# Performance work log

Hardware: AMD Instinct MI355X
Metric: run time of the kernel (lower is better)

Reference implementation:

```python
import jax, jax.numpy as jnp
import numpy as np

N_A, N_P, N_T = 40000, 100000, 20000
D = 128
OUT = 64
E_AP, E_PT = 500000, 800000


def setup_inputs() -> dict:
    key = jax.random.key(0)
    ks = jax.random.split(key, 24)
    s = 1.0 / np.sqrt(D)
    inp = {
        'x_author': jax.random.normal(ks[0], (N_A, D), jnp.float32),
        'x_paper': jax.random.normal(ks[1], (N_P, D), jnp.float32),
        'x_term': jax.random.normal(ks[2], (N_T, D), jnp.float32),
        'W_l': jax.random.normal(ks[3], (3, 2, 4, D, D), jnp.float32) * s,
        'b_l': jax.random.normal(ks[4], (3, 2, 4, D), jnp.float32) * 0.01,
        'W_r': jax.random.normal(ks[5], (3, 2, 4, D, D), jnp.float32) * s,
        'lin_model_W': jax.random.normal(ks[6], (D, OUT), jnp.float32) * s,
        'lin_model_b': jax.random.normal(ks[7], (OUT,), jnp.float32) * 0.01,
        'lin_temp_W': jax.random.normal(ks[8], (D, OUT), jnp.float32) * s,
        'lin_temp_b': jax.random.normal(ks[9], (OUT,), jnp.float32) * 0.01,
        'lin2_W': jax.random.normal(ks[10], (OUT, 1), jnp.float32) * (1.0 / np.sqrt(OUT)),
        'lin2_b': jnp.ones((1,), jnp.float32),
        'src_ap': jax.random.randint(ks[11], (E_AP,), 0, N_A, jnp.int32),
        'dst_ap': jax.random.randint(ks[12], (E_AP,), 0, N_P, jnp.int32),
        'src_pa': jax.random.randint(ks[13], (E_AP,), 0, N_P, jnp.int32),
        'dst_pa': jax.random.randint(ks[14], (E_AP,), 0, N_A, jnp.int32),
        'src_pt': jax.random.randint(ks[15], (E_PT,), 0, N_P, jnp.int32),
        'dst_pt': jax.random.randint(ks[16], (E_PT,), 0, N_T, jnp.int32),
        'src_tp': jax.random.randint(ks[17], (E_PT,), 0, N_T, jnp.int32),
        'dst_tp': jax.random.randint(ks[18], (E_PT,), 0, N_P, jnp.int32),
    }
    return inp


def _sage(x_src, x_dst, src, dst, n_dst, Wl, bl, Wr):
    # PyG SAGEConv: lin_l(mean_aggr(x_j)) + lin_r(x_dst); lin_r has no bias.
    xj = x_src[src]                                         # [E, D] gather
    ssum = jax.ops.segment_sum(xj, dst, num_segments=n_dst)  # [n_dst, D]
    cnt = jax.ops.segment_sum(jnp.ones((src.shape[0],), x_src.dtype), dst,
                              num_segments=n_dst)
    mean = ssum / jnp.maximum(cnt, 1.0)[:, None]
    return mean @ Wl + bl + x_dst @ Wr


def _hetero_stack(xa, xp, xt, Wl, bl, Wr, edges, relu=True):
    # Wl/bl/Wr: [num_layers, 4, ...]; relation order: a->p, p->a, p->t, t->p.
    (sap, dap, spa, dpa, spt, dpt, stp, dtp) = edges
    n_layers = Wl.shape[0]
    for l in range(n_layers):
        p_new = (_sage(xa, xp, sap, dap, N_P, Wl[l, 0], bl[l, 0], Wr[l, 0])
                 + _sage(xt, xp, stp, dtp, N_P, Wl[l, 3], bl[l, 3], Wr[l, 3]))
        a_new = _sage(xp, xa, spa, dpa, N_A, Wl[l, 1], bl[l, 1], Wr[l, 1])
        t_new = _sage(xp, xt, spt, dpt, N_T, Wl[l, 2], bl[l, 2], Wr[l, 2])
        xa, xp, xt = jax.nn.relu(a_new), jax.nn.relu(p_new), jax.nn.relu(t_new)
    return xa, xp, xt


def reference(x_author, x_paper, x_term, W_l, b_l, W_r,
              lin_model_W, lin_model_b, lin_temp_W, lin_temp_b,
              lin2_W, lin2_b,
              src_ap, dst_ap, src_pa, dst_pa, src_pt, dst_pt, src_tp, dst_tp):
    edges = (src_ap, dst_ap, src_pa, dst_pa, src_pt, dst_pt, src_tp, dst_tp)
    # stack 0: self.model (DBLP) on raw features
    ma, mp, mt = _hetero_stack(x_author, x_paper, x_term,
                               W_l[0], b_l[0], W_r[0], edges)
    logits = ma @ lin_model_W + lin_model_b                  # [N_A, OUT]
    # stack 1: graph_temperature_scale (DBLP) on model's hidden x_dict
    ta, tp_, tt = _hetero_stack(ma, mp, mt, W_l[1], b_l[1], W_r[1], edges)
    ll1 = ta @ lin_temp_W + lin_temp_b                       # [N_A, OUT]
    temperature = ll1 @ lin2_W + lin2_b                      # [N_A, 1]
    # stack 2: self.convs on raw features (dropout = identity in eval mode)
    oa, op, ot = _hetero_stack(x_author, x_paper, x_term,
                               W_l[2], b_l[2], W_r[2], edges)
    return logits / temperature, oa, op, ot
```

## Files before the change

### kernel.cpp

```cpp
#include <hip/hip_runtime.h>
#include <cstdint>

#define N_A 40000
#define N_P 100000
#define N_T 20000
#define D 128
#define OUT_DIM 64
#define E_AP 500000
#define E_PT 800000

typedef __attribute__((ext_vector_type(8))) short bf16x8;
typedef __attribute__((ext_vector_type(4))) float f32x4;

static inline int ceil_div(int a, int b){ return (a + b - 1) / b; }

__device__ inline unsigned short f2bf(float f){
  uint32_t u = __builtin_bit_cast(uint32_t, f);
  uint32_t r = (u + 0x7FFFu + ((u >> 16) & 1u)) >> 16;
  return (unsigned short)r;
}
__device__ inline float bf2f(unsigned short h){
  uint32_t u = ((uint32_t)h) << 16;
  return __builtin_bit_cast(float, u);
}

__global__ void hist_kernel(const int* __restrict__ dst, int E, int* __restrict__ cnt){
  int i = blockIdx.x * blockDim.x + threadIdx.x;
  if (i < E) atomicAdd(&cnt[dst[i]], 1);
}

__global__ void block_sums_kernel(const int* __restrict__ cnt, int n, int* __restrict__ bsums){
  __shared__ int red[256];
  int b = blockIdx.x, t = threadIdx.x;
  int base = b * 1024;
  int s = 0;
  for (int i = t; i < 1024; i += 256){ int idx = base + i; if (idx < n) s += cnt[idx]; }
  red[t] = s; __syncthreads();
  for (int off = 128; off > 0; off >>= 1){ if (t < off) red[t] += red[t + off]; __syncthreads(); }
  if (t == 0) bsums[b] = red[0];
}

__global__ void scan_bsums_kernel(int* bsums, int nb){
  __shared__ int sh[128];
  int t = threadIdx.x;
  int v = (t < nb) ? bsums[t] : 0;
  sh[t] = v; __syncthreads();
  int inc = v;
  for (int off = 1; off < 128; off <<= 1){
    int x = (t >= off) ? sh[t - off] : 0; __syncthreads();
    inc += x; sh[t] = inc; __syncthreads();
  }
  if (t < nb) bsums[t] = inc - v;
}

__global__ void scan_final_kernel(const int* __restrict__ cnt, int n, const int* __restrict__ bsums,
                                  int* __restrict__ rowptr, int E){
  __shared__ int sh[256];
  int b = blockIdx.x, t = threadIdx.x;
  int base = b * 1024 + t * 4;
  int v[4]; int s = 0;
  #pragma unroll
  for (int j = 0; j < 4; j++){ int idx = base + j; v[j] = (idx < n) ? cnt[idx] : 0; s += v[j]; }
  sh[t] = s; __syncthreads();
  int inc = s;
  for (int off = 1; off < 256; off <<= 1){
    int x = (t >= off) ? sh[t - off] : 0; __syncthreads();
    inc += x; sh[t] = inc; __syncthreads();
  }
  int run = inc - s + bsums[b];
  #pragma unroll
  for (int j = 0; j < 4; j++){ int idx = base + j; if (idx < n) rowptr[idx] = run; run += v[j]; }
  if (b == 0 && t == 0) rowptr[n] = E;
}

__global__ void cursor_inv_kernel(const int* __restrict__ rowptr, const int* __restrict__ cnt,
                                  int n, int* __restrict__ cursor, float* __restrict__ inv){
  int i = blockIdx.x * blockDim.x + threadIdx.x;
  if (i < n){
    cursor[i] = rowptr[i];
    int c = cnt[i];
    inv[i] = 1.0f / (float)(c > 0 ? c : 1);
  }
}

__global__ void fill_kernel(const int* __restrict__ src, const int* __restrict__ dst, int E,
                            int* __restrict__ cursor, int* __restrict__ eidx){
  int i = blockIdx.x * blockDim.x + threadIdx.x;
  if (i < E){
    int d = dst[i];
    int pos = atomicAdd(&cursor[d], 1);
    eidx[pos] = src[i];
  }
}

__global__ void combine_wr_kernel(const float* __restrict__ Wr, float* __restrict__ wrc){
  int i = blockIdx.x * blockDim.x + threadIdx.x;
  if (i < 6 * D * D){
    int sl = i >> 14; int off = i & (D * D - 1);
    wrc[i] = Wr[(size_t)(sl * 4 + 0) * D * D + off] + Wr[(size_t)(sl * 4 + 3) * D * D + off];
  }
}

__global__ void combine_bias_kernel(const float* __restrict__ bl, float* __restrict__ bcomb){
  int i = blockIdx.x * blockDim.x + threadIdx.x;
  if (i < 6 * D){
    int sl = i >> 7; int off = i & (D - 1);
    bcomb[i] = bl[(size_t)(sl * 4 + 0) * D + off] + bl[(size_t)(sl * 4 + 3) * D + off];
  }
}

__global__ __launch_bounds__(256)
void pack_weights_kernel(const float* __restrict__ W_l, const float* __restrict__ W_r,
                         const float* __restrict__ wrc, const float* __restrict__ linW,
                         unsigned short* __restrict__ packs){
  int id = blockIdx.x;
  const float* src; int N = 128;
  if (id < 24)      src = W_l + (size_t)id * 16384;
  else if (id < 48) src = W_r + (size_t)(id - 24) * 16384;
  else if (id < 54) src = wrc + (size_t)(id - 48) * 16384;
  else            { src = linW; N = 64; }
  unsigned short* dhi = packs + (size_t)id * 32768;
  unsigned short* dlo = dhi + 16384;
  int ncf = N / 16;
  int slots = 4 * ncf * 64;
  for (int s = threadIdx.x; s < slots; s += 256){
    int frag = s >> 6, l = s & 63;
    int kc = frag / ncf, cf = frag - kc * ncf;
    int kb = kc * 32 + ((l >> 4) * 8);
    int col = cf * 16 + (l & 15);
    bf16x8 hv, lv;
    #pragma unroll
    for (int i = 0; i < 8; ++i){
      float f = src[(size_t)(kb + i) * N + col];
      unsigned short h = f2bf(f);
      hv[i] = (short)h;
      lv[i] = (short)f2bf(f - bf2f(h));
    }
    *(bf16x8*)(dhi + (size_t)s * 8) = hv;
    *(bf16x8*)(dlo + (size_t)s * 8) = lv;
  }
}

__global__ __launch_bounds__(256)
void agg_mean_kernel(const int* __restrict__ rowptr, const int* __restrict__ eidx,
                     const float* __restrict__ inv, const float* __restrict__ xsrc,
                     float* __restrict__ out, int ndst){
  int w = (blockIdx.x * blockDim.x + threadIdx.x) >> 6;
  if (w >= ndst) return;
  int l = threadIdx.x & 63;
  int p = l >> 5, kk = l & 31;
  int beg = rowptr[w], end = rowptr[w + 1];
  float4 a0 = make_float4(0,0,0,0), a1 = make_float4(0,0,0,0);
  float4 a2 = make_float4(0,0,0,0), a3 = make_float4(0,0,0,0);
  int e = beg;
  for (; e + 8 <= end; e += 8){
    int s0 = eidx[e + p], s1 = eidx[e + 2 + p], s2 = eidx[e + 4 + p], s3 = eidx[e + 6 + p];
    float4 v0 = ((const float4*)(xsrc + (size_t)s0 * D))[kk];
    float4 v1 = ((const float4*)(xsrc + (size_t)s1 * D))[kk];
    float4 v2 = ((const float4*)(xsrc + (size_t)s2 * D))[kk];
    float4 v3 = ((const float4*)(xsrc + (size_t)s3 * D))[kk];
    a0.x += v0.x; a0.y += v0.y; a0.z += v0.z; a0.w += v0.w;
    a1.x += v1.x; a1.y += v1.y; a1.z += v1.z; a1.w += v1.w;
    a2.x += v2.x; a2.y += v2.y; a2.z += v2.z; a2.w += v2.w;
    a3.x += v3.x; a3.y += v3.y; a3.z += v3.z; a3.w += v3.w;
  }
  if (e + 4 <= end){
    int s0 = eidx[e + p], s1 = eidx[e + 2 + p];
    float4 v0 = ((const float4*)(xsrc + (size_t)s0 * D))[kk];
    float4 v1 = ((const float4*)(xsrc + (size_t)s1 * D))[kk];
    a0.x += v0.x; a0.y += v0.y; a0.z += v0.z; a0.w += v0.w;
    a1.x += v1.x; a1.y += v1.y; a1.z += v1.z; a1.w += v1.w;
    e += 4;
  }
  if (e + 2 <= end){
    int s0 = eidx[e + p];
    float4 v0 = ((const float4*)(xsrc + (size_t)s0 * D))[kk];
    a0.x += v0.x; a0.y += v0.y; a0.z += v0.z; a0.w += v0.w;
    e += 2;
  }
  if (e < end && p == 0){
    int s0 = eidx[e];
    float4 v0 = ((const float4*)(xsrc + (size_t)s0 * D))[kk];
    a0.x += v0.x; a0.y += v0.y; a0.z += v0.z; a0.w += v0.w;
  }
  a0.x += a1.x + a2.x + a3.x; a0.y += a1.y + a2.y + a3.y;
  a0.z += a1.z + a2.z + a3.z; a0.w += a1.w + a2.w + a3.w;
  a0.x += __shfl_xor(a0.x, 32); a0.y += __shfl_xor(a0.y, 32);
  a0.z += __shfl_xor(a0.z, 32); a0.w += __shfl_xor(a0.w, 32);
  if (p == 0){
    float iv = inv[w];
    float4 r; r.x = a0.x * iv; r.y = a0.y * iv; r.z = a0.z * iv; r.w = a0.w * iv;
    ((float4*)(out + (size_t)w * D))[kk] = r;
  }
}

template<int NIN, int NCFT, bool RELU, bool DIV>
__global__ __launch_bounds__(256)
void gemm_mfma(const float* __restrict__ in0, const unsigned short* hi0, const unsigned short* lo0,
               const float* __restrict__ in1, const unsigned short* hi1, const unsigned short* lo1,
               const float* __restrict__ in2, const unsigned short* hi2, const unsigned short* lo2,
               const float* __restrict__ bias, const float* __restrict__ tdiv,
               float* __restrict__ out, int nrows){
  constexpr int WC = NCFT / 4;
  constexpr int WR = 4 / WC;
  const int tid    = threadIdx.x;
  const int w      = tid >> 6;
  const int l      = tid & 63;
  const int lane15 = l & 15;
  const int colg   = l >> 4;
  const int wr     = w / WC, wc = w % WC;
  const int rbase  = blockIdx.x * (WR * 64) + wr * 64;

  f32x4 acc[4][4];
  #pragma unroll
  for (int m = 0; m < 4; ++m)
    #pragma unroll
    for (int cf = 0; cf < 4; ++cf) acc[m][cf] = (f32x4){0.f, 0.f, 0.f, 0.f};

  const float* ins[3]          = {in0, in1, in2};
  const unsigned short* his[3] = {hi0, hi1, hi2};
  const unsigned short* los[3] = {lo0, lo1, lo2};

  #pragma unroll
  for (int inp = 0; inp < NIN; ++inp){
    const float* A = ins[inp];
    const bf16x8* WH = (const bf16x8*)his[inp];
    const bf16x8* WL = (const bf16x8*)los[inp];
    #pragma unroll
    for (int kc = 0; kc < 4; ++kc){
      bf16x8 bh[4], bl[4];
      #pragma unroll
      for (int cf = 0; cf < 4; ++cf){
        int idx = (kc * NCFT + wc * 4 + cf) * 64 + l;
        bh[cf] = WH[idx];
        bl[cf] = WL[idx];
      }
      bf16x8 ah[4], al[4];
      #pragma unroll
      for (int m = 0; m < 4; ++m){
        int gr = rbase + m * 16 + lane15; if (gr >= nrows) gr = nrows - 1;
        const float4* p = (const float4*)(A + (size_t)gr * 128 + kc * 32 + colg * 8);
        float4 v0 = p[0], v1 = p[1];
        float fs[8] = {v0.x, v0.y, v0.z, v0.w, v1.x, v1.y, v1.z, v1.w};
        #pragma unroll
        for (int i = 0; i < 8; ++i){
          uint32_t u = __builtin_bit_cast(uint32_t, fs[i]);
          unsigned short h = (unsigned short)(u >> 16);
          float r = fs[i] - __builtin_bit_cast(float, u & 0xFFFF0000u);
          ah[m][i] = (short)h;
          al[m][i] = (short)(__builtin_bit_cast(uint32_t, r) >> 16);
        }
      }
      #pragma unroll
      for (int cf = 0; cf < 4; ++cf){
        #pragma unroll
        for (int m = 0; m < 4; ++m){
          acc[m][cf] = __builtin_amdgcn_mfma_f32_16x16x32_bf16(ah[m], bh[cf], acc[m][cf], 0, 0, 0);
          acc[m][cf] = __builtin_amdgcn_mfma_f32_16x16x32_bf16(al[m], bh[cf], acc[m][cf], 0, 0, 0);
          acc[m][cf] = __builtin_amdgcn_mfma_f32_16x16x32_bf16(ah[m], bl[cf], acc[m][cf], 0, 0, 0);
        }
      }
    }
  }

  #pragma unroll
  for (int cf = 0; cf < 4; ++cf){
    int col = (wc * 4 + cf) * 16 + lane15;
    float bv = bias[col];
    #pragma unroll
    for (int m = 0; m < 4; ++m){
      #pragma unroll
      for (int i = 0; i < 4; ++i){
        int gr = rbase + m * 16 + colg * 4 + i;
        if (gr < nrows){
          float v = acc[m][cf][i] + bv;
          if (RELU) v = fmaxf(v, 0.f);
          if (DIV)  v = v / tdiv[gr];
          out[(size_t)gr * (NCFT * 16) + col] = v;
        }
      }
    }
  }
}

__global__ void wtc_kernel(const float* __restrict__ Wt, const float* __restrict__ bt,
                           const float* __restrict__ W2, const float* __restrict__ b2,
                           float* __restrict__ wtc){
  int k = threadIdx.x;
  if (k < 128){
    float s = 0.f;
    #pragma unroll 4
    for (int j = 0; j < 64; ++j) s += Wt[k * 64 + j] * W2[j];
    wtc[k] = s;
  }
  if (k == 0){
    float s = 0.f;
    for (int j = 0; j < 64; ++j) s += bt[j] * W2[j];
    wtc[128] = s + b2[0];
  }
}

__global__ __launch_bounds__(256)
void temp_kernel(const float* __restrict__ ta, const float* __restrict__ wtc,
                 float* __restrict__ temp, int n){
  int w = (blockIdx.x * blockDim.x + threadIdx.x) >> 6;
  if (w >= n) return;
  int l = threadIdx.x & 63;
  float2 v = ((const float2*)(ta + (size_t)w * D))[l];
  float2 c = ((const float2*)wtc)[l];
  float s = v.x * c.x + v.y * c.y;
  #pragma unroll
  for (int off = 32; off > 0; off >>= 1) s += __shfl_xor(s, off);
  if (l == 0) temp[w] = s + wtc[128];
}

extern "C" void kernel_launch(void* const* d_in, const int* in_sizes, int n_in,
                              void* d_out, int out_size, void* d_ws, size_t ws_size,
                              hipStream_t stream){
  const float* x_author    = (const float*)d_in[0];
  const float* x_paper     = (const float*)d_in[1];
  const float* x_term      = (const float*)d_in[2];
  const float* W_l         = (const float*)d_in[3];
  const float* b_l         = (const float*)d_in[4];
  const float* W_r         = (const float*)d_in[5];
  const float* lin_model_W = (const float*)d_in[6];
  const float* lin_model_b = (const float*)d_in[7];
  const float* lin_temp_W  = (const float*)d_in[8];
  const float* lin_temp_b  = (const float*)d_in[9];
  const float* lin2_W      = (const float*)d_in[10];
  const float* lin2_b      = (const float*)d_in[11];
  const int* src_ap = (const int*)d_in[12];
  const int* dst_ap = (const int*)d_in[13];
  const int* src_pa = (const int*)d_in[14];
  const int* dst_pa = (const int*)d_in[15];
  const int* src_pt = (const int*)d_in[16];
  const int* dst_pt = (const int*)d_in[17];
  const int* src_tp = (const int*)d_in[18];
  const int* dst_tp = (const int*)d_in[19];

  char* wp = (char*)d_ws;
  auto alloc = [&](size_t bytes)->void*{
    void* r = (void*)wp; wp += (bytes + 255) & ~(size_t)255; return r;
  };
  int*   rowptr_ap = (int*)alloc((N_P + 1) * 4);
  int*   cnt_ap    = (int*)alloc(N_P * 4);
  int*   cur_ap    = (int*)alloc(N_P * 4);
  int*   eidx_ap   = (int*)alloc((size_t)E_AP * 4);
  float* inv_ap    = (float*)alloc(N_P * 4);
  int*   rowptr_pa = (int*)alloc((N_A + 1) * 4);
  int*   cnt_pa    = (int*)alloc(N_A * 4);
  int*   cur_pa    = (int*)alloc(N_A * 4);
  int*   eidx_pa   = (int*)alloc((size_t)E_AP * 4);
  float* inv_pa    = (float*)alloc(N_A * 4);
  int*   rowptr_pt = (int*)alloc((N_T + 1) * 4);
  int*   cnt_pt    = (int*)alloc(N_T * 4);
  int*   cur_pt    = (int*)alloc(N_T * 4);
  int*   eidx_pt   = (int*)alloc((size_t)E_PT * 4);
  float* inv_pt    = (float*)alloc(N_T * 4);
  int*   rowptr_tp = (int*)alloc((N_P + 1) * 4);
  int*   cnt_tp    = (int*)alloc(N_P * 4);
  int*   cur_tp    = (int*)alloc(N_P * 4);
  int*   eidx_tp   = (int*)alloc((size_t)E_PT * 4);
  float* inv_tp    = (float*)alloc(N_P * 4);
  int*   bsums     = (int*)alloc(1024 * 4);
  unsigned short* packs = (unsigned short*)alloc((size_t)55 * 32768 * 2);
  float* wrc   = (float*)alloc((size_t)6 * D * D * 4);
  float* bcomb = (float*)alloc((size_t)6 * D * 4);
  float* wtc   = (float*)alloc(129 * 4);
  float* temp  = (float*)alloc((size_t)N_A * 4);
  float* gA  = (float*)alloc((size_t)N_A * D * 4);
  float* gP1 = (float*)alloc((size_t)N_P * D * 4);
  float* gP2 = (float*)alloc((size_t)N_P * D * 4);
  float* gT  = (float*)alloc((size_t)N_T * D * 4);
  float* A1 = (float*)alloc((size_t)N_A * D * 4);
  float* P1 = (float*)alloc((size_t)N_P * D * 4);
  float* T1 = (float*)alloc((size_t)N_T * D * 4);
  float* A2 = (float*)alloc((size_t)N_A * D * 4);
  float* P2 = (float*)alloc((size_t)N_P * D * 4);
  float* T2 = (float*)alloc((size_t)N_T * D * 4);
  float* A0 = A2;
  float* P0 = P2;
  float* T0 = T2;
  float* TA = P2;

  auto build = [&](const int* src, const int* dst, int E, int n,
                   int* rowptr, int* cnt, int* cursor, int* eidx, float* inv){
    hipMemsetAsync(cnt, 0, (size_t)n * 4, stream);
    hist_kernel<<<ceil_div(E, 256), 256, 0, stream>>>(dst, E, cnt);
    int nb = ceil_div(n, 1024);
    block_sums_kernel<<<nb, 256, 0, stream>>>(cnt, n, bsums);
    scan_bsums_kernel<<<1, 128, 0, stream>>>(bsums, nb);
    scan_final_kernel<<<nb, 256, 0, stream>>>(cnt, n, bsums, rowptr, E);
    cursor_inv_kernel<<<ceil_div(n, 256), 256, 0, stream>>>(rowptr, cnt, n, cursor, inv);
    fill_kernel<<<ceil_div(E, 256), 256, 0, stream>>>(src, dst, E, cursor, eidx);
  };
  build(src_ap, dst_ap, E_AP, N_P, rowptr_ap, cnt_ap, cur_ap, eidx_ap, inv_ap);
  build(src_pa, dst_pa, E_AP, N_A, rowptr_pa, cnt_pa, cur_pa, eidx_pa, inv_pa);
  build(src_pt, dst_pt, E_PT, N_T, rowptr_pt, cnt_pt, cur_pt, eidx_pt, inv_pt);
  build(src_tp, dst_tp, E_PT, N_P, rowptr_tp, cnt_tp, cur_tp, eidx_tp, inv_tp);

  combine_wr_kernel<<<ceil_div(6 * D * D, 256), 256, 0, stream>>>(W_r, wrc);
  combine_bias_kernel<<<ceil_div(6 * D, 256), 256, 0, stream>>>(b_l, bcomb);
  pack_weights_kernel<<<55, 256, 0, stream>>>(W_l, W_r, wrc, lin_model_W, packs);
  wtc_kernel<<<1, 128, 0, stream>>>(lin_temp_W, lin_temp_b, lin2_W, lin2_b, wtc);

  auto HI = [&](int id){ return packs + (size_t)id * 32768; };
  auto LO = [&](int id){ return packs + (size_t)id * 32768 + 16384; };
  auto IDL = [&](int s, int l, int r){ return (s * 2 + l) * 4 + r; };
  auto IDR = [&](int s, int l, int r){ return 24 + (s * 2 + l) * 4 + r; };
  auto IDC = [&](int s, int l){ return 48 + s * 2 + l; };
  auto Bl  = [&](int s, int l, int r){ return b_l + (size_t)((s * 2 + l) * 4 + r) * D; };
  auto BC  = [&](int s, int l){ return bcomb + (size_t)(s * 2 + l) * D; };

  auto agg = [&](const int* rowptr, const int* eidx, const float* inv,
                 const float* xsrc, float* outp, int ndst){
    agg_mean_kernel<<<ceil_div(ndst, 4), 256, 0, stream>>>(rowptr, eidx, inv, xsrc, outp, ndst);
  };

  auto agg_all = [&](const float* ia, const float* ip, const float* it){
    agg(rowptr_ap, eidx_ap, inv_ap, ia, gP1, N_P);
    agg(rowptr_tp, eidx_tp, inv_tp, it, gP2, N_P);
    agg(rowptr_pa, eidx_pa, inv_pa, ip, gA, N_A);
    agg(rowptr_pt, eidx_pt, inv_pt, ip, gT, N_T);
  };

  auto gemms = [&](const float* ia, const float* ip, const float* it, int s, int l,
                   float* oa, float* op, float* ot){
    if (op) gemm_mfma<3, 8, true, false><<<ceil_div(N_P, 128), 256, 0, stream>>>(
        gP1, HI(IDL(s, l, 0)), LO(IDL(s, l, 0)),
        gP2, HI(IDL(s, l, 3)), LO(IDL(s, l, 3)),
        ip,  HI(IDC(s, l)),    LO(IDC(s, l)),
        BC(s, l), nullptr, op, N_P);
    if (oa) gemm_mfma<2, 8, true, false><<<ceil_div(N_A, 128), 256, 0, stream>>>(
        gA, HI(IDL(s, l, 1)), LO(IDL(s, l, 1)),
        ia, HI(IDR(s, l, 1)), LO(IDR(s, l, 1)),
        nullptr, nullptr, nullptr,
        Bl(s, l, 1), nullptr, oa, N_A);
    if (ot) gemm_mfma<2, 8, true, false><<<ceil_div(N_T, 128), 256, 0, stream>>>(
        gT, HI(IDL(s, l, 2)), LO(IDL(s, l, 2)),
        it, HI(IDR(s, l, 2)), LO(IDR(s, l, 2)),
        nullptr, nullptr, nullptr,
        Bl(s, l, 2), nullptr, ot, N_T);
  };

  float* out_logits = (float*)d_out;
  float* out_oa = out_logits + (size_t)N_A * OUT_DIM;
  float* out_op = out_oa + (size_t)N_A * D;
  float* out_ot = out_op + (size_t)N_P * D;

  agg_all(x_author, x_paper, x_term);
  gemms(x_author, x_paper, x_term, 0, 0, A1, P1, T1);
  gemms(x_author, x_paper, x_term, 2, 0, A2, P2, T2);
  agg_all(A2, P2, T2);
  gemms(A2, P2, T2, 2, 1, out_oa, out_op, out_ot);
  agg_all(A1, P1, T1);
  gemms(A1, P1, T1, 0, 1, A0, P0, T0);
  agg_all(A0, P0, T0);
  gemms(A0, P0, T0, 1, 0, A1, P1, T1);
  agg(rowptr_pa, eidx_pa, inv_pa, P1, gA, N_A);
  gemm_mfma<2, 8, true, false><<<ceil_div(N_A, 128), 256, 0, stream>>>(
      gA, HI(IDL(1, 1, 1)), LO(IDL(1, 1, 1)),
      A1, HI(IDR(1, 1, 1)), LO(IDR(1, 1, 1)),
      nullptr, nullptr, nullptr,
      Bl(1, 1, 1), nullptr, TA, N_A);
  temp_kernel<<<ceil_div(N_A, 4), 256, 0, stream>>>(TA, wtc, temp, N_A);
  gemm_mfma<1, 4, false, true><<<ceil_div(N_A, 256), 256, 0, stream>>>(
      A0, HI(54), LO(54),
      nullptr, nullptr, nullptr,
      nullptr, nullptr, nullptr,
      lin_model_b, temp, out_logits, N_A);
}
```

Baseline: 2.158 ms.

## Store intermediates as split bf16 hi/lo planes and narrow aggregation to 16 lanes

Intermediate activations and aggregated means are now stored as two bf16 planes (hi and residual lo) rather than fp32. The GEMM then loads the MFMA operands directly instead of splitting fp32 values on every tile load. The aggregation kernel now gives each destination row to 16 lanes that each handle 8 columns, and the GEMM row tile per warp (MF) is reduced for the smaller node types. Bytes moved per gather stay the same, since two bf16 planes equal one fp32 row, but they come as two separate 16-byte reads. The hi/lo split also loses a little precision, and the bf16-to-float conversion work moves into the gather loop.

```diff
diff --git a/kernel.cpp b/kernel.cpp
--- a/kernel.cpp
+++ b/kernel.cpp
@@ -22,6 +22,13 @@
 __device__ inline float bf2f(unsigned short h){
   uint32_t u = ((uint32_t)h) << 16;
   return __builtin_bit_cast(float, u);
+}
+__device__ inline uint32_t tsplit_pack(float v){
+  uint32_t u = __builtin_bit_cast(uint32_t, v);
+  uint32_t h = u >> 16;
+  float rem = v - __builtin_bit_cast(float, u & 0xFFFF0000u);
+  uint32_t l = f2bf(rem);
+  return h | (l << 16);
 }
 
 __global__ void hist_kernel(const int* __restrict__ dst, int E, int* __restrict__ cnt){
@@ -141,66 +148,76 @@
   }
 }
 
+__device__ inline void addrow_f32(const float* __restrict__ base, int s, int c, float* acc){
+  const float4* p = (const float4*)(base + (size_t)s * D + c * 8);
+  float4 a = p[0], b = p[1];
+  acc[0] += a.x; acc[1] += a.y; acc[2] += a.z; acc[3] += a.w;
+  acc[4] += b.x; acc[5] += b.y; acc[6] += b.z; acc[7] += b.w;
+}
+__device__ inline void addrow_bf(const unsigned short* __restrict__ H,
+                                 const unsigned short* __restrict__ L, int s, int c, float* acc){
+  bf16x8 h = *(const bf16x8*)(H + (size_t)s * D + c * 8);
+  bf16x8 l = *(const bf16x8*)(L + (size_t)s * D + c * 8);
+  #pragma unroll
+  for (int i = 0; i < 8; ++i)
+    acc[i] += bf2f((unsigned short)h[i]) + bf2f((unsigned short)l[i]);
+}
+
+template<bool SRCF32>
 __global__ __launch_bounds__(256)
 void agg_mean_kernel(const int* __restrict__ rowptr, const int* __restrict__ eidx,
-                     const float* __restrict__ inv, const float* __restrict__ xsrc,
-                     float* __restrict__ out, int ndst){
-  int w = (blockIdx.x * blockDim.x + threadIdx.x) >> 6;
-  if (w >= ndst) return;
-  int l = threadIdx.x & 63;
-  int p = l >> 5, kk = l & 31;
-  int beg = rowptr[w], end = rowptr[w + 1];
-  float4 a0 = make_float4(0,0,0,0), a1 = make_float4(0,0,0,0);
-  float4 a2 = make_float4(0,0,0,0), a3 = make_float4(0,0,0,0);
+                     const float* __restrict__ inv,
+                     const void* __restrict__ srcHv, const void* __restrict__ srcLv,
+                     unsigned short* __restrict__ dstH, unsigned short* __restrict__ dstL,
+                     int ndst){
+  int g = (blockIdx.x * blockDim.x + threadIdx.x) >> 4;
+  if (g >= ndst) return;
+  int c = threadIdx.x & 15;
+  int beg = rowptr[g], end = rowptr[g + 1];
+  float acc[8];
+  #pragma unroll
+  for (int i = 0; i < 8; ++i) acc[i] = 0.f;
+  const float* F = (const float*)srcHv;
+  const unsigned short* H = (const unsigned short*)srcHv;
+  const unsigned short* L = (const unsigned short*)srcLv;
   int e = beg;
-  for (; e + 8 <= end; e += 8){
-    int s0 = eidx[e + p], s1 = eidx[e + 2 + p], s2 = eidx[e + 4 + p], s3 = eidx[e + 6 + p];
-    float4 v0 = ((const float4*)(xsrc + (size_t)s0 * D))[kk];
-    float4 v1 = ((const float4*)(xsrc + (size_t)s1 * D))[kk];
-    float4 v2 = ((const float4*)(xsrc + (size_t)s2 * D))[kk];
-    float4 v3 = ((const float4*)(xsrc + (size_t)s3 * D))[kk];
-    a0.x += v0.x; a0.y += v0.y; a0.z += v0.z; a0.w += v0.w;
-    a1.x += v1.x; a1.y += v1.y; a1.z += v1.z; a1.w += v1.w;
-    a2.x += v2.x; a2.y += v2.y; a2.z += v2.z; a2.w += v2.w;
-    a3.x += v3.x; a3.y += v3.y; a3.z += v3.z; a3.w += v3.w;
-  }
-  if (e + 4 <= end){
-    int s0 = eidx[e + p], s1 = eidx[e + 2 + p];
-    float4 v0 = ((const float4*)(xsrc + (size_t)s0 * D))[kk];
-    float4 v1 = ((const float4*)(xsrc + (size_t)s1 * D))[kk];
-    a0.x += v0.x; a0.y += v0.y; a0.z += v0.z; a0.w += v0.w;
-    a1.x += v1.x; a1.y += v1.y; a1.z += v1.z; a1.w += v1.w;
-    e += 4;
-  }
-  if (e + 2 <= end){
-    int s0 = eidx[e + p];
-    float4 v0 = ((const float4*)(xsrc + (size_t)s0 * D))[kk];
-    a0.x += v0.x; a0.y += v0.y; a0.z += v0.z; a0.w += v0.w;
-    e += 2;
-  }
-  if (e < end && p == 0){
+  for (; e + 4 <= end; e += 4){
+    int s0 = eidx[e], s1 = eidx[e + 1], s2 = eidx[e + 2], s3 = eidx[e + 3];
+    if (SRCF32){
+      addrow_f32(F, s0, c, acc); addrow_f32(F, s1, c, acc);
+      addrow_f32(F, s2, c, acc); addrow_f32(F, s3, c, acc);
+    } else {
+      addrow_bf(H, L, s0, c, acc); addrow_bf(H, L, s1, c, acc);
+      addrow_bf(H, L, s2, c, acc); addrow_bf(H, L, s3, c, acc);
+    }
+  }
+  for (; e < end; ++e){
     int s0 = eidx[e];
-    float4 v0 = ((const float4*)(xsrc + (size_t)s0 * D))[kk];
-    a0.x += v0.x; a0.y += v0.y; a0.z += v0.z; a0.w += v0.w;
-  }
-  a0.x += a1.x + a2.x + a3.x; a0.y += a1.y + a2.y + a3.y;
-  a0.z += a1.z + a2.z + a3.z; a0.w += a1.w + a2.w + a3.w;
-  a0.x += __shfl_xor(a0.x, 32); a0.y += __shfl_xor(a0.y, 32);
-  a0.z += __shfl_xor(a0.z, 32); a0.w += __shfl_xor(a0.w, 32);
-  if (p == 0){
-    float iv = inv[w];
-    float4 r; r.x = a0.x * iv; r.y = a0.y * iv; r.z = a0.z * iv; r.w = a0.w * iv;
-    ((float4*)(out + (size_t)w * D))[kk] = r;
-  }
-}
-
-template<int NIN, int NCFT, bool RELU, bool DIV>
+    if (SRCF32) addrow_f32(F, s0, c, acc);
+    else        addrow_bf(H, L, s0, c, acc);
+  }
+  float iv = inv[g];
+  bf16x8 hv, lv;
+  #pragma unroll
+  for (int i = 0; i < 8; ++i){
+    uint32_t pk = tsplit_pack(acc[i] * iv);
+    hv[i] = (short)(pk & 0xFFFF);
+    lv[i] = (short)(pk >> 16);
+  }
+  *(bf16x8*)(dstH + (size_t)g * D + c * 8) = hv;
+  *(bf16x8*)(dstL + (size_t)g * D + c * 8) = lv;
+}
+
+template<int NIN, int F32MASK, int NCFT, int MF, bool RELU, bool DIV, bool OUT32>
 __global__ __launch_bounds__(256)
-void gemm_mfma(const float* __restrict__ in0, const unsigned short* hi0, const unsigned short* lo0,
-               const float* __restrict__ in1, const unsigned short* hi1, const unsigned short* lo1,
-               const float* __restrict__ in2, const unsigned short* hi2, const unsigned short* lo2,
+void gemm_mfma(const void* __restrict__ aH0, const unsigned short* __restrict__ aL0,
+               const unsigned short* __restrict__ wH0, const unsigned short* __restrict__ wL0,
+               const void* __restrict__ aH1, const unsigned short* __restrict__ aL1,
+               const unsigned short* __restrict__ wH1, const unsigned short* __restrict__ wL1,
+               const void* __restrict__ aH2, const unsigned short* __restrict__ aL2,
+               const unsigned short* __restrict__ wH2, const unsigned short* __restrict__ wL2,
                const float* __restrict__ bias, const float* __restrict__ tdiv,
-               float* __restrict__ out, int nrows){
+               void* __restrict__ outp, size_t out_lo_off, int nrows){
   constexpr int WC = NCFT / 4;
   constexpr int WR = 4 / WC;
   const int tid    = threadIdx.x;
@@ -209,23 +226,23 @@
   const int lane15 = l & 15;
   const int colg   = l >> 4;
   const int wr     = w / WC, wc = w % WC;
-  const int rbase  = blockIdx.x * (WR * 64) + wr * 64;
-
-  f32x4 acc[4][4];
-  #pragma unroll
-  for (int m = 0; m < 4; ++m)
+  const int rbase  = blockIdx.x * (WR * MF * 16) + wr * (MF * 16);
+
+  f32x4 acc[MF][4];
+  #pragma unroll
+  for (int m = 0; m < MF; ++m)
     #pragma unroll
     for (int cf = 0; cf < 4; ++cf) acc[m][cf] = (f32x4){0.f, 0.f, 0.f, 0.f};
 
-  const float* ins[3]          = {in0, in1, in2};
-  const unsigned short* his[3] = {hi0, hi1, hi2};
-  const unsigned short* los[3] = {lo0, lo1, lo2};
+  const void* aHs[3]           = {aH0, aH1, aH2};
+  const unsigned short* aLs[3] = {aL0, aL1, aL2};
+  const unsigned short* wHs[3] = {wH0, wH1, wH2};
+  const unsigned short* wLs[3] = {wL0, wL1, wL2};
 
   #pragma unroll
   for (int inp = 0; inp < NIN; ++inp){
-    const float* A = ins[inp];
-    const bf16x8* WH = (const bf16x8*)his[inp];
-    const bf16x8* WL = (const bf16x8*)los[inp];
+    const bf16x8* WH = (const bf16x8*)wHs[inp];
+    const bf16x8* WL = (const bf16x8*)wLs[inp];
     #pragma unroll
     for (int kc = 0; kc < 4; ++kc){
       bf16x8 bh[4], bl[4];
@@ -235,26 +252,33 @@
         bh[cf] = WH[idx];
         bl[cf] = WL[idx];
       }
-      bf16x8 ah[4], al[4];
+      bf16x8 ah[MF], al[MF];
       #pragma unroll
-      for (int m = 0; m < 4; ++m){
+      for (int m = 0; m < MF; ++m){
         int gr = rbase + m * 16 + lane15; if (gr >= nrows) gr = nrows - 1;
-        const float4* p = (const float4*)(A + (size_t)gr * 128 + kc * 32 + colg * 8);
-        float4 v0 = p[0], v1 = p[1];
-        float fs[8] = {v0.x, v0.y, v0.z, v0.w, v1.x, v1.y, v1.z, v1.w};
-        #pragma unroll
-        for (int i = 0; i < 8; ++i){
-          uint32_t u = __builtin_bit_cast(uint32_t, fs[i]);
-          unsigned short h = (unsigned short)(u >> 16);
-          float r = fs[i] - __builtin_bit_cast(float, u & 0xFFFF0000u);
-          ah[m][i] = (short)h;
-          al[m][i] = (short)(__builtin_bit_cast(uint32_t, r) >> 16);
+        if ((F32MASK >> inp) & 1){
+          const float* Af = (const float*)aHs[inp];
+          const float4* p = (const float4*)(Af + (size_t)gr * 128 + kc * 32 + colg * 8);
+          float4 v0 = p[0], v1 = p[1];
+          float fs[8] = {v0.x, v0.y, v0.z, v0.w, v1.x, v1.y, v1.z, v1.w};
+          #pragma unroll
+          for (int i = 0; i < 8; ++i){
+            uint32_t pk = tsplit_pack(fs[i]);
+            ah[m][i] = (short)(pk & 0xFFFF);
+            al[m][i] = (short)(pk >> 16);
+          }
+        } else {
+          const unsigned short* AH = (const unsigned short*)aHs[inp];
+          const unsigned short* AL = aLs[inp];
+          size_t idx = (size_t)gr * 128 + kc * 32 + colg * 8;
+          ah[m] = *(const bf16x8*)(AH + idx);
+          al[m] = *(const bf16x8*)(AL + idx);
         }
       }
       #pragma unroll
       for (int cf = 0; cf < 4; ++cf){
         #pragma unroll
-        for (int m = 0; m < 4; ++m){
+        for (int m = 0; m < MF; ++m){
           acc[m][cf] = __builtin_amdgcn_mfma_f32_16x16x32_bf16(ah[m], bh[cf], acc[m][cf], 0, 0, 0);
           acc[m][cf] = __builtin_amdgcn_mfma_f32_16x16x32_bf16(al[m], bh[cf], acc[m][cf], 0, 0, 0);
           acc[m][cf] = __builtin_amdgcn_mfma_f32_16x16x32_bf16(ah[m], bl[cf], acc[m][cf], 0, 0, 0);
@@ -268,7 +292,7 @@
     int col = (wc * 4 + cf) * 16 + lane15;
     float bv = bias[col];
     #pragma unroll
-    for (int m = 0; m < 4; ++m){
+    for (int m = 0; m < MF; ++m){
       #pragma unroll
       for (int i = 0; i < 4; ++i){
         int gr = rbase + m * 16 + colg * 4 + i;
@@ -276,7 +300,14 @@
           float v = acc[m][cf][i] + bv;
           if (RELU) v = fmaxf(v, 0.f);
           if (DIV)  v = v / tdiv[gr];
-          out[(size_t)gr * (NCFT * 16) + col] = v;
+          size_t oi = (size_t)gr * (NCFT * 16) + col;
+          if (OUT32){
+            ((float*)outp)[oi] = v;
+          } else {
+            uint32_t pk = tsplit_pack(v);
+            ((unsigned short*)outp)[oi] = (unsigned short)(pk & 0xFFFF);
+            ((unsigned short*)outp)[out_lo_off + oi] = (unsigned short)(pk >> 16);
+          }
         }
       }
     }
@@ -301,18 +332,21 @@
 }
 
 __global__ __launch_bounds__(256)
-void temp_kernel(const float* __restrict__ ta, const float* __restrict__ wtc,
-                 float* __restrict__ temp, int n){
+void temp_kernel(const unsigned short* __restrict__ taH, const unsigned short* __restrict__ taL,
+                 const float* __restrict__ wtc, float* __restrict__ temp, int n){
   int w = (blockIdx.x * blockDim.x + threadIdx.x) >> 6;
   if (w >= n) return;
   int l = threadIdx.x & 63;
-  float2 v = ((const float2*)(ta + (size_t)w * D))[l];
+  ushort2 h = *(const ushort2*)(taH + (size_t)w * D + 2 * l);
+  ushort2 lo = *(const ushort2*)(taL + (size_t)w * D + 2 * l);
   float2 c = ((const float2*)wtc)[l];
-  float s = v.x * c.x + v.y * c.y;
+  float s = (bf2f(h.x) + bf2f(lo.x)) * c.x + (bf2f(h.y) + bf2f(lo.y)) * c.y;
   #pragma unroll
   for (int off = 32; off > 0; off >>= 1) s += __shfl_xor(s, off);
   if (l == 0) temp[w] = s + wtc[128];
 }
+
+struct Split { unsigned short* h; unsigned short* l; };
 
 extern "C" void kernel_launch(void* const* d_in, const int* in_sizes, int n_in,
                               void* d_out, int out_size, void* d_ws, size_t ws_size,
@@ -341,6 +375,10 @@
   char* wp = (char*)d_ws;
   auto alloc = [&](size_t bytes)->void*{
     void* r = (void*)wp; wp += (bytes + 255) & ~(size_t)255; return r;
+  };
+  auto mkSplit = [&](int n)->Split{
+    unsigned short* p = (unsigned short*)alloc((size_t)n * D * 4);
+    return {p, p + (size_t)n * D};
   };
   int*   rowptr_ap = (int*)alloc((N_P + 1) * 4);
   int*   cnt_ap    = (int*)alloc(N_P * 4);
@@ -368,24 +406,15 @@
   float* bcomb = (float*)alloc((size_t)6 * D * 4);
   float* wtc   = (float*)alloc(129 * 4);
   float* temp  = (float*)alloc((size_t)N_A * 4);
-  float* gA  = (float*)alloc((size_t)N_A * D * 4);
-  float* gP1 = (float*)alloc((size_t)N_P * D * 4);
-  float* gP2 = (float*)alloc((size_t)N_P * D * 4);
-  float* gT  = (float*)alloc((size_t)N_T * D * 4);
-  float* A1 = (float*)alloc((size_t)N_A * D * 4);
-  float* P1 = (float*)alloc((size_t)N_P * D * 4);
-  float* T1 = (float*)alloc((size_t)N_T * D * 4);
-  float* A2 = (float*)alloc((size_t)N_A * D * 4);
-  float* P2 = (float*)alloc((size_t)N_P * D * 4);
-  float* T2 = (float*)alloc((size_t)N_T * D * 4);
-  float* A0 = A2;
-  float* P0 = P2;
-  float* T0 = T2;
-  float* TA = P2;
+  Split gA = mkSplit(N_A), gP1 = mkSplit(N_P), gP2 = mkSplit(N_P), gT = mkSplit(N_T);
+  Split A1 = mkSplit(N_A), P1 = mkSplit(N_P), T1 = mkSplit(N_T);
+  Split A2 = mkSplit(N_A), P2 = mkSplit(N_P), T2 = mkSplit(N_T);
+  Split A0 = A2, P0 = P2, T0 = T2;
+  Split TA = P2;
 
   auto build = [&](const int* src, const int* dst, int E, int n,
                    int* rowptr, int* cnt, int* cursor, int* eidx, float* inv){
-    hipMemsetAsync(cnt, 0, (size_t)n * 4, stream);
+    (void)hipMemsetAsync(cnt, 0, (size_t)n * 4, stream);
     hist_kernel<<<ceil_div(E, 256), 256, 0, stream>>>(dst, E, cnt);
     int nb = ceil_div(n, 1024);
     block_sums_kernel<<<nb, 256, 0, stream>>>(cnt, n, bsums);
@@ -412,35 +441,81 @@
   auto Bl  = [&](int s, int l, int r){ return b_l + (size_t)((s * 2 + l) * 4 + r) * D; };
   auto BC  = [&](int s, int l){ return bcomb + (size_t)(s * 2 + l) * D; };
 
-  auto agg = [&](const int* rowptr, const int* eidx, const float* inv,
-                 const float* xsrc, float* outp, int ndst){
-    agg_mean_kernel<<<ceil_div(ndst, 4), 256, 0, stream>>>(rowptr, eidx, inv, xsrc, outp, ndst);
-  };
-
-  auto agg_all = [&](const float* ia, const float* ip, const float* it){
-    agg(rowptr_ap, eidx_ap, inv_ap, ia, gP1, N_P);
-    agg(rowptr_tp, eidx_tp, inv_tp, it, gP2, N_P);
-    agg(rowptr_pa, eidx_pa, inv_pa, ip, gA, N_A);
-    agg(rowptr_pt, eidx_pt, inv_pt, ip, gT, N_T);
-  };
-
-  auto gemms = [&](const float* ia, const float* ip, const float* it, int s, int l,
-                   float* oa, float* op, float* ot){
-    if (op) gemm_mfma<3, 8, true, false><<<ceil_div(N_P, 128), 256, 0, stream>>>(
-        gP1, HI(IDL(s, l, 0)), LO(IDL(s, l, 0)),
-        gP2, HI(IDL(s, l, 3)), LO(IDL(s, l, 3)),
-        ip,  HI(IDC(s, l)),    LO(IDC(s, l)),
-        BC(s, l), nullptr, op, N_P);
-    if (oa) gemm_mfma<2, 8, true, false><<<ceil_div(N_A, 128), 256, 0, stream>>>(
-        gA, HI(IDL(s, l, 1)), LO(IDL(s, l, 1)),
-        ia, HI(IDR(s, l, 1)), LO(IDR(s, l, 1)),
-        nullptr, nullptr, nullptr,
-        Bl(s, l, 1), nullptr, oa, N_A);
-    if (ot) gemm_mfma<2, 8, true, false><<<ceil_div(N_T, 128), 256, 0, stream>>>(
-        gT, HI(IDL(s, l, 2)), LO(IDL(s, l, 2)),
-        it, HI(IDR(s, l, 2)), LO(IDR(s, l, 2)),
-        nullptr, nullptr, nullptr,
-        Bl(s, l, 2), nullptr, ot, N_T);
+  auto aggB = [&](const int* rowptr, const int* eidx, const float* inv,
+                  Split src, Split dst, int ndst){
+    agg_mean_kernel<false><<<ceil_div(ndst, 16), 256, 0, stream>>>(
+        rowptr, eidx, inv, (const void*)src.h, (const void*)src.l, dst.h, dst.l, ndst);
+  };
+  auto aggF = [&](const int* rowptr, const int* eidx, const float* inv,
+                  const float* src, Split dst, int ndst){
+    agg_mean_kernel<true><<<ceil_div(ndst, 16), 256, 0, stream>>>(
+        rowptr, eidx, inv, (const void*)src, nullptr, dst.h, dst.l, ndst);
+  };
+
+  auto agg_all = [&](Split ia, Split ip, Split it){
+    aggB(rowptr_ap, eidx_ap, inv_ap, ia, gP1, N_P);
+    aggB(rowptr_tp, eidx_tp, inv_tp, it, gP2, N_P);
+    aggB(rowptr_pa, eidx_pa, inv_pa, ip, gA, N_A);
+    aggB(rowptr_pt, eidx_pt, inv_pt, ip, gT, N_T);
+  };
+
+  auto gemms_l0 = [&](int s, Split oa, Split op, Split ot){
+    gemm_mfma<3, 4, 8, 4, true, false, false><<<ceil_div(N_P, 128), 256, 0, stream>>>(
+        (const void*)gP1.h, gP1.l, HI(IDL(s, 0, 0)), LO(IDL(s, 0, 0)),
+        (const void*)gP2.h, gP2.l, HI(IDL(s, 0, 3)), LO(IDL(s, 0, 3)),
+        (const void*)x_paper, nullptr, HI(IDC(s, 0)), LO(IDC(s, 0)),
+        BC(s, 0), nullptr, (void*)op.h, (size_t)(op.l - op.h), N_P);
+    gemm_mfma<2, 2, 8, 2, true, false, false><<<ceil_div(N_A, 64), 256, 0, stream>>>(
+        (const void*)gA.h, gA.l, HI(IDL(s, 0, 1)), LO(IDL(s, 0, 1)),
+        (const void*)x_author, nullptr, HI(IDR(s, 0, 1)), LO(IDR(s, 0, 1)),
+        nullptr, nullptr, nullptr, nullptr,
+        Bl(s, 0, 1), nullptr, (void*)oa.h, (size_t)(oa.l - oa.h), N_A);
+    gemm_mfma<2, 2, 8, 2, true, false, false><<<ceil_div(N_T, 64), 256, 0, stream>>>(
+        (const void*)gT.h, gT.l, HI(IDL(s, 0, 2)), LO(IDL(s, 0, 2)),
+        (const void*)x_term, nullptr, HI(IDR(s, 0, 2)), LO(IDR(s, 0, 2)),
+        nullptr, nullptr, nullptr, nullptr,
+        Bl(s, 0, 2), nullptr, (void*)ot.h, (size_t)(ot.l - ot.h), N_T);
+  };
+
+  auto gemms = [&](Split ia, Split ip, Split it, int s, int l,
+                   Split* oa, Split* op, Split* ot,
+                   float* oa32, float* op32, float* ot32){
+    if (op || op32){
+      if (op) gemm_mfma<3, 0, 8, 4, true, false, false><<<ceil_div(N_P, 128), 256, 0, stream>>>(
+          (const void*)gP1.h, gP1.l, HI(IDL(s, l, 0)), LO(IDL(s, l, 0)),
+          (const void*)gP2.h, gP2.l, HI(IDL(s, l, 3)), LO(IDL(s, l, 3)),
+          (const void*)ip.h,  ip.l,  HI(IDC(s, l)),    LO(IDC(s, l)),
+          BC(s, l), nullptr, (void*)op->h, (size_t)(op->l - op->h), N_P);
+      else gemm_mfma<3, 0, 8, 4, true, false, true><<<ceil_div(N_P, 128), 256, 0, stream>>>(
+          (const void*)gP1.h, gP1.l, HI(IDL(s, l, 0)), LO(IDL(s, l, 0)),
+          (const void*)gP2.h, gP2.l, HI(IDL(s, l, 3)), LO(IDL(s, l, 3)),
+          (const void*)ip.h,  ip.l,  HI(IDC(s, l)),    LO(IDC(s, l)),
+          BC(s, l), nullptr, (void*)op32, 0, N_P);
+    }
+    if (oa || oa32){
+      if (oa) gemm_mfma<2, 0, 8, 2, true, false, false><<<ceil_div(N_A, 64), 256, 0, stream>>>(
+          (const void*)gA.h, gA.l, HI(IDL(s, l, 1)), LO(IDL(s, l, 1)),
+          (const void*)ia.h, ia.l, HI(IDR(s, l, 1)), LO(IDR(s, l, 1)),
+          nullptr, nullptr, nullptr, nullptr,
+          Bl(s, l, 1), nullptr, (void*)oa->h, (size_t)(oa->l - oa->h), N_A);
+      else gemm_mfma<2, 0, 8, 2, true, false, true><<<ceil_div(N_A, 64), 256, 0, stream>>>(
+          (const void*)gA.h, gA.l, HI(IDL(s, l, 1)), LO(IDL(s, l, 1)),
+          (const void*)ia.h, ia.l, HI(IDR(s, l, 1)), LO(IDR(s, l, 1)),
+          nullptr, nullptr, nullptr, nullptr,
+          Bl(s, l, 1), nullptr, (void*)oa32, 0, N_A);
+    }
+    if (ot || ot32){
+      if (ot) gemm_mfma<2, 0, 8, 2, true, false, false><<<ceil_div(N_T, 64), 256, 0, stream>>>(
+          (const void*)gT.h, gT.l, HI(IDL(s, l, 2)), LO(IDL(s, l, 2)),
+          (const void*)it.h, it.l, HI(IDR(s, l, 2)), LO(IDR(s, l, 2)),
+          nullptr, nullptr, nullptr, nullptr,
+          Bl(s, l, 2), nullptr, (void*)ot->h, (size_t)(ot->l - ot->h), N_T);
+      else gemm_mfma<2, 0, 8, 2, true, false, true><<<ceil_div(N_T, 64), 256, 0, stream>>>(
+          (const void*)gT.h, gT.l, HI(IDL(s, l, 2)), LO(IDL(s, l, 2)),
+          (const void*)it.h, it.l, HI(IDR(s, l, 2)), LO(IDR(s, l, 2)),
+          nullptr, nullptr, nullptr, nullptr,
+          Bl(s, l, 2), nullptr, (void*)ot32, 0, N_T);
+    }
   };
 
   float* out_logits = (float*)d_out;
@@ -448,25 +523,28 @@
   float* out_op = out_oa + (size_t)N_A * D;
   float* out_ot = out_op + (size_t)N_P * D;
 
-  agg_all(x_author, x_paper, x_term);
-  gemms(x_author, x_paper, x_term, 0, 0, A1, P1, T1);
-  gemms(x_author, x_paper, x_term, 2, 0, A2, P2, T2);
+  aggF(rowptr_ap, eidx_ap, inv_ap, x_author, gP1, N_P);
+  aggF(rowptr_tp, eidx_tp, inv_tp, x_term,   gP2, N_P);
+  aggF(rowptr_pa, eidx_pa, inv_pa, x_paper,  gA,  N_A);
+  aggF(rowptr_pt, eidx_pt, inv_pt, x_paper,  gT,  N_T);
+  gemms_l0(0, A1, P1, T1);
+  gemms_l0(2, A2, P2, T2);
   agg_all(A2, P2, T2);
-  gemms(A2, P2, T2, 2, 1, out_oa, out_op, out_ot);
+  gemms(A2, P2, T2, 2, 1, nullptr, nullptr, nullptr, out_oa, out_op, out_ot);
   agg_all(A1, P1, T1);
-  gemms(A1, P1, T1, 0, 1, A0, P0, T0);
+  gemms(A1, P1, T1, 0, 1, &A0, &P0, &T0, nullptr, nullptr, nullptr);
   agg_all(A0, P0, T0);
-  gemms(A0, P0, T0, 1, 0, A1, P1, T1);
-  agg(rowptr_pa, eidx_pa, inv_pa, P1, gA, N_A);
-  gemm_mfma<2, 8, true, false><<<ceil_div(N_A, 128), 256, 0, stream>>>(
-      gA, HI(IDL(1, 1, 1)), LO(IDL(1, 1, 1)),
-      A1, HI(IDR(1, 1, 1)), LO(IDR(1, 1, 1)),
-      nullptr, nullptr, nullptr,
-      Bl(1, 1, 1), nullptr, TA, N_A);
-  temp_kernel<<<ceil_div(N_A, 4), 256, 0, stream>>>(TA, wtc, temp, N_A);
-  gemm_mfma<1, 4, false, true><<<ceil_div(N_A, 256), 256, 0, stream>>>(
-      A0, HI(54), LO(54),
-      nullptr, nullptr, nullptr,
-      nullptr, nullptr, nullptr,
-      lin_model_b, temp, out_logits, N_A);
-}
+  gemms(A0, P0, T0, 1, 0, &A1, &P1, &T1, nullptr, nullptr, nullptr);
+  aggB(rowptr_pa, eidx_pa, inv_pa, P1, gA, N_A);
+  gemm_mfma<2, 0, 8, 2, true, false, false><<<ceil_div(N_A, 64), 256, 0, stream>>>(
+      (const void*)gA.h, gA.l, HI(IDL(1, 1, 1)), LO(IDL(1, 1, 1)),
+      (const void*)A1.h, A1.l, HI(IDR(1, 1, 1)), LO(IDR(1, 1, 1)),
+      nullptr, nullptr, nullptr, nullptr,
+      Bl(1, 1, 1), nullptr, (void*)TA.h, (size_t)(TA.l - TA.h), N_A);
+  temp_kernel<<<ceil_div(N_A, 4), 256, 0, stream>>>(TA.h, TA.l, wtc, temp, N_A);
+  gemm_mfma<1, 0, 4, 2, false, true, true><<<ceil_div(N_A, 128), 256, 0, stream>>>(
+      (const void*)A0.h, A0.l, HI(54), LO(54),
+      nullptr, nullptr, nullptr, nullptr,
+      nullptr, nullptr, nullptr, nullptr,
+      lin_model_b, temp, (void*)out_logits, 0, N_A);
+}
```

Result: no change. 2.169 ms (+0.5%).
